# Performance work log

Measured on AMD Instinct MI355X. Metric: run time of the kernel, lower is better.

Reference implementation:

```python
import jax, jax.numpy as jnp
import numpy as np

B, S, H, L, V = 128, 512, 1024, 4, 32000


def setup_inputs() -> dict:
    key = jax.random.key(0)
    ks = jax.random.split(key, 7)
    lengths = jax.random.randint(ks[0], (B,), 1, S + 1)
    lengths = lengths.at[0].set(S)  # force max length == S so T is static
    tok = jax.random.randint(ks[1], (B, S), 1, V)  # nonzero tokens inside length
    pos = jnp.arange(S)[None, :]
    x = jnp.where(pos < lengths[:, None], tok, 0)  # 0 = pad (x>0 defines length)
    emb = jax.random.normal(ks[2], (V, H), dtype=jnp.float32) * 0.02
    W_ih = jax.random.normal(ks[3], (L, 4 * H, H), dtype=jnp.float32) / np.float32(np.sqrt(H))
    W_hh = jax.random.normal(ks[4], (L, 4 * H, H), dtype=jnp.float32) / np.float32(np.sqrt(H))
    b_ih = jax.random.normal(ks[5], (L, 4 * H), dtype=jnp.float32) * 0.01
    b_hh = jax.random.normal(ks[6], (L, 4 * H), dtype=jnp.float32) * 0.01
    return {"x": x, "emb": emb, "W_ih": W_ih, "W_hh": W_hh, "b_ih": b_ih, "b_hh": b_hh}


def reference(x, emb, W_ih, W_hh, b_ih, b_hh):
    # lengths and pack's descending sort (pack_padded_sequence, enforce_sorted=False)
    lengths = jnp.sum(x > 0, axis=1)                         # [B]
    sorted_idx = jnp.argsort(-lengths, stable=True)          # sorted (desc) order
    unsort_idx = jnp.argsort(sorted_idx)                     # packed.unsorted_indices

    # Source bug: `start` is never advanced, so every iteration runs a ONE-step
    # stacked LSTM (zero init state) on packed.data[0:bs_t] == t=0 embeddings of
    # the bs_t longest sequences. Compute that single step once on all rows.
    xt = emb[x[sorted_idx, 0]]                               # [B, H] sorted order
    h0 = jnp.zeros_like(xt)                                  # zero initial hidden
    hs, cs = [], []
    for l in range(W_ih.shape[0]):
        gates = xt @ W_ih[l].T + b_ih[l] + h0 @ W_hh[l].T + b_hh[l]
        i, f, g, o = jnp.split(gates, 4, axis=-1)            # torch LSTMCell order
        c = jax.nn.sigmoid(i) * jnp.tanh(g)                  # f * c0 = 0
        h = jax.nn.sigmoid(o) * jnp.tanh(c)
        xt = h
        hs.append(h)
        cs.append(c)

    # output[t, b] = top-layer h for original seq b, zeroed where t >= lengths[b]
    T = x.shape[1]                                           # max length == S
    h_top = xt[unsort_idx]                                   # back to original order
    tmask = (jnp.arange(T)[:, None] < lengths[None, :]).astype(h_top.dtype)  # [T,B]
    output = tmask[:, :, None] * h_top[None, :, :]           # [T, B, H]

    # state from the LAST loop iteration: sorted order, rows >= bs_last zero-padded
    bs_last = jnp.sum(lengths >= T)                          # batch size at t = T-1
    smask = (jnp.arange(x.shape[0]) < bs_last).astype(h_top.dtype)[None, :, None]
    state_h = jnp.stack(hs, axis=0) * smask                  # [L, B, H]
    state_c = jnp.stack(cs, axis=0) * smask                  # [L, B, H]
    return output, state_h, state_c
```

## Files before the change

kernel.cpp:

```cpp
#include <hip/hip_runtime.h>

#define Bn 128
#define Sn 512
#define Hn 1024
#define Ln 4

typedef float nfloat4 __attribute__((ext_vector_type(4)));

__device__ __forceinline__ float sigmoidf_(float x) { return 1.0f / (1.0f + __expf(-x)); }

__global__ __launch_bounds__(128) void len_kernel(const int* __restrict__ x, int* __restrict__ lengths) {
  const int b = blockIdx.x, t = threadIdx.x;
  int4 v = ((const int4*)x)[b * 128 + t];
  int c = (v.x > 0) + (v.y > 0) + (v.z > 0) + (v.w > 0);
  for (int off = 32; off > 0; off >>= 1) c += __shfl_down(c, off);
  __shared__ int tmp[2];
  if ((t & 63) == 0) tmp[t >> 6] = c;
  __syncthreads();
  if (t == 0) lengths[b] = tmp[0] + tmp[1];
}

__global__ __launch_bounds__(128) void sort_kernel(const int* __restrict__ x, const int* __restrict__ lengths,
                                                   int* __restrict__ rank, int* __restrict__ tok_sorted,
                                                   int* __restrict__ bs_last) {
  __shared__ int sl[128];
  __shared__ int cnt;
  const int b = threadIdx.x;
  const int len = lengths[b];
  sl[b] = len;
  if (b == 0) cnt = 0;
  __syncthreads();
  int r = 0;
  for (int b2 = 0; b2 < 128; b2++) {
    int l2 = sl[b2];
    r += (l2 > len) || (l2 == len && b2 < b);
  }
  rank[b] = r;
  tok_sorted[r] = x[b * Sn];
  if (len >= Sn) atomicAdd(&cnt, 1);
  __syncthreads();
  if (b == 0) bs_last[0] = cnt;
}

__global__ __launch_bounds__(256) void gather_kernel(const int* __restrict__ tok_sorted,
                                                     const float* __restrict__ emb,
                                                     float* __restrict__ xt0) {
  const int r = blockIdx.x;
  const int tok = tok_sorted[r];
  ((float4*)xt0)[r * 256 + threadIdx.x] = ((const float4*)emb)[(size_t)tok * 256 + threadIdx.x];
}

__global__ __launch_bounds__(256) void gemm_kernel(const float* __restrict__ xt,
                                                   const float* __restrict__ Wl,
                                                   float* __restrict__ part) {
  __shared__ float xtT[32][132];
  __shared__ float Ws[32][96];
  const int t = threadIdx.x;
  const int mtile = blockIdx.x & 31;
  const int kc = blockIdx.x >> 5;
  const int rg = t & 31;
  const int msub = t >> 5;
  const int k0 = kc * 128;

  float acc[3][4][4];
#pragma unroll
  for (int q = 0; q < 3; q++)
#pragma unroll
    for (int mm = 0; mm < 4; mm++)
#pragma unroll
      for (int rr = 0; rr < 4; rr++) acc[q][mm][rr] = 0.0f;

  float4 xreg[4], wreg[3];
  {
    const int kt = k0;
#pragma unroll
    for (int i = 0; i < 4; i++) {
      int vi = i * 256 + t, r = vi >> 3, kv = vi & 7;
      xreg[i] = *(const float4*)&xt[r * 1024 + kt + kv * 4];
    }
#pragma unroll
    for (int i = 0; i < 3; i++) {
      int vi = i * 256 + t, jj = vi >> 3, kv = vi & 7;
      int q = jj >> 5, mloc = jj & 31;
      int qoff = (q == 0) ? 0 : ((q == 1) ? 2048 : 3072);
      wreg[i] = *(const float4*)&Wl[(size_t)(qoff + mtile * 32 + mloc) * 1024 + kt + kv * 4];
    }
  }

#pragma unroll
  for (int tile = 0; tile < 4; tile++) {
    __syncthreads();
#pragma unroll
    for (int i = 0; i < 4; i++) {
      int vi = i * 256 + t, r = vi >> 3, kv = vi & 7;
      xtT[kv * 4 + 0][r] = xreg[i].x;
      xtT[kv * 4 + 1][r] = xreg[i].y;
      xtT[kv * 4 + 2][r] = xreg[i].z;
      xtT[kv * 4 + 3][r] = xreg[i].w;
    }
#pragma unroll
    for (int i = 0; i < 3; i++) {
      int vi = i * 256 + t, jj = vi >> 3, kv = vi & 7;
      Ws[kv * 4 + 0][jj] = wreg[i].x;
      Ws[kv * 4 + 1][jj] = wreg[i].y;
      Ws[kv * 4 + 2][jj] = wreg[i].z;
      Ws[kv * 4 + 3][jj] = wreg[i].w;
    }
    float4 xnxt[4], wnxt[3];
    if (tile < 3) {
      const int kt = k0 + (tile + 1) * 32;
#pragma unroll
      for (int i = 0; i < 4; i++) {
        int vi = i * 256 + t, r = vi >> 3, kv = vi & 7;
        xnxt[i] = *(const float4*)&xt[r * 1024 + kt + kv * 4];
      }
#pragma unroll
      for (int i = 0; i < 3; i++) {
        int vi = i * 256 + t, jj = vi >> 3, kv = vi & 7;
        int q = jj >> 5, mloc = jj & 31;
        int qoff = (q == 0) ? 0 : ((q == 1) ? 2048 : 3072);
        wnxt[i] = *(const float4*)&Wl[(size_t)(qoff + mtile * 32 + mloc) * 1024 + kt + kv * 4];
      }
    }
    __syncthreads();
#pragma unroll
    for (int kk = 0; kk < 32; kk++) {
      const float4 xv = *(const float4*)&xtT[kk][rg * 4];
      const float4 w0 = *(const float4*)&Ws[kk][msub * 4];
      const float4 w1 = *(const float4*)&Ws[kk][32 + msub * 4];
      const float4 w2 = *(const float4*)&Ws[kk][64 + msub * 4];
      const float xa[4] = {xv.x, xv.y, xv.z, xv.w};
      const float wv[3][4] = {{w0.x, w0.y, w0.z, w0.w},
                              {w1.x, w1.y, w1.z, w1.w},
                              {w2.x, w2.y, w2.z, w2.w}};
#pragma unroll
      for (int q = 0; q < 3; q++)
#pragma unroll
        for (int mm = 0; mm < 4; mm++)
#pragma unroll
          for (int rr = 0; rr < 4; rr++)
            acc[q][mm][rr] = fmaf(wv[q][mm], xa[rr], acc[q][mm][rr]);
    }
    if (tile < 3) {
#pragma unroll
      for (int i = 0; i < 4; i++) xreg[i] = xnxt[i];
#pragma unroll
      for (int i = 0; i < 3; i++) wreg[i] = wnxt[i];
    }
  }

  const int mbase = mtile * 32 + msub * 4;
#pragma unroll
  for (int q = 0; q < 3; q++)
#pragma unroll
    for (int mm = 0; mm < 4; mm++) {
      float4 v = make_float4(acc[q][mm][0], acc[q][mm][1], acc[q][mm][2], acc[q][mm][3]);
      *(float4*)&part[(((size_t)kc * 3 + q) * 1024 + (mbase + mm)) * 128 + rg * 4] = v;
    }
}

__global__ __launch_bounds__(256) void act_kernel(const float* __restrict__ part,
                                                  const float* __restrict__ bih,
                                                  const float* __restrict__ bhh,
                                                  const int* __restrict__ bs_last,
                                                  float* __restrict__ xt_out,
                                                  float* __restrict__ sh,
                                                  float* __restrict__ sc) {
  __shared__ float hT[128][17];
  __shared__ float cT[128][17];
  const int t = threadIdx.x;
  const int m0 = blockIdx.x * 16;
  const int bs = bs_last[0];
#pragma unroll
  for (int i = 0; i < 8; i++) {
    int e = i * 256 + t;
    int r = e & 127;
    int mloc = e >> 7;
    int m = m0 + mloc;
    float si = 0.f, sg = 0.f, so = 0.f;
#pragma unroll
    for (int kc = 0; kc < 8; kc++) {
      si += part[(((size_t)kc * 3 + 0) * 1024 + m) * 128 + r];
      sg += part[(((size_t)kc * 3 + 1) * 1024 + m) * 128 + r];
      so += part[(((size_t)kc * 3 + 2) * 1024 + m) * 128 + r];
    }
    si += bih[m] + bhh[m];
    sg += bih[2048 + m] + bhh[2048 + m];
    so += bih[3072 + m] + bhh[3072 + m];
    float c = sigmoidf_(si) * tanhf(sg);
    float h = sigmoidf_(so) * tanhf(c);
    hT[r][mloc] = h;
    cT[r][mloc] = c;
  }
  __syncthreads();
#pragma unroll
  for (int i = 0; i < 8; i++) {
    int e = i * 256 + t;
    int mloc = e & 15;
    int r = e >> 4;
    float h = hT[r][mloc];
    float c = cT[r][mloc];
    float msk = (r < bs) ? 1.0f : 0.0f;
    xt_out[r * 1024 + m0 + mloc] = h;
    sh[r * 1024 + m0 + mloc] = msk * h;
    sc[r * 1024 + m0 + mloc] = msk * c;
  }
}

__global__ __launch_bounds__(256) void bcast_kernel(const float* __restrict__ hfin,
                                                    const int* __restrict__ lengths,
                                                    const int* __restrict__ rank,
                                                    float* __restrict__ out) {
  const int b = blockIdx.x & 127;
  const int tp = blockIdx.x >> 7;
  const int len = lengths[b];
  nfloat4 v = (nfloat4)0.0f;
  if (tp < len) {
    const int r = rank[b];
    v = ((const nfloat4*)hfin)[r * 256 + threadIdx.x];
  }
  __builtin_nontemporal_store(v, &((nfloat4*)out)[(size_t)blockIdx.x * 256 + threadIdx.x]);
}

extern "C" void kernel_launch(void* const* d_in, const int* in_sizes, int n_in,
                              void* d_out, int out_size, void* d_ws, size_t ws_size,
                              hipStream_t stream) {
  const int* x = (const int*)d_in[0];
  const float* emb = (const float*)d_in[1];
  const float* W_ih = (const float*)d_in[2];
  const float* b_ih = (const float*)d_in[4];
  const float* b_hh = (const float*)d_in[5];

  float* out = (float*)d_out;
  float* sh = out + (size_t)Sn * Bn * Hn;
  float* sc = sh + (size_t)Ln * Bn * Hn;
  float* part = out;

  char* ws = (char*)d_ws;
  int* lengths = (int*)ws;
  int* rank = lengths + 128;
  int* tok_sorted = rank + 128;
  int* bs_last = tok_sorted + 128;
  float* xtA = (float*)(ws + 4096);
  float* xtB = xtA + 128 * 1024;

  len_kernel<<<128, 128, 0, stream>>>(x, lengths);
  sort_kernel<<<1, 128, 0, stream>>>(x, lengths, rank, tok_sorted, bs_last);
  gather_kernel<<<128, 256, 0, stream>>>(tok_sorted, emb, xtA);

  float* xin = xtA;
  float* xout = xtB;
  for (int l = 0; l < Ln; l++) {
    gemm_kernel<<<256, 256, 0, stream>>>(xin, W_ih + (size_t)l * 4 * Hn * Hn, part);
    act_kernel<<<64, 256, 0, stream>>>(part, b_ih + l * 4 * Hn, b_hh + l * 4 * Hn, bs_last,
                                       xout, sh + (size_t)l * Bn * Hn, sc + (size_t)l * Bn * Hn);
    float* tmp = xin; xin = xout; xout = tmp;
  }
  bcast_kernel<<<Sn * Bn, 256, 0, stream>>>(xin, lengths, rank, out);
}
```

Measured before the change: 521.2 us.

## Fuse embedding gather into first GEMM, simplify act kernel, coarsen broadcast

Drops the separate gather kernel: the first layer's GEMM reads embedding rows directly through a token index cached in shared memory. The activation kernel becomes one thread per batch row handling four hidden units, with float4 stores and no shared-memory transpose. The broadcast kernel goes from one block per (t,b) to 1024 blocks that each write 64 timesteps in a loop. Together these cut launch count and per-block overhead, at the cost of less parallelism per block in the act and broadcast kernels.

```diff
diff --git a/kernel.cpp b/kernel.cpp
--- a/kernel.cpp
+++ b/kernel.cpp
@@ -42,25 +42,32 @@
   if (b == 0) bs_last[0] = cnt;
 }
 
-__global__ __launch_bounds__(256) void gather_kernel(const int* __restrict__ tok_sorted,
-                                                     const float* __restrict__ emb,
-                                                     float* __restrict__ xt0) {
-  const int r = blockIdx.x;
-  const int tok = tok_sorted[r];
-  ((float4*)xt0)[r * 256 + threadIdx.x] = ((const float4*)emb)[(size_t)tok * 256 + threadIdx.x];
-}
-
 __global__ __launch_bounds__(256) void gemm_kernel(const float* __restrict__ xt,
+                                                   const int* __restrict__ tok,
                                                    const float* __restrict__ Wl,
                                                    float* __restrict__ part) {
   __shared__ float xtT[32][132];
   __shared__ float Ws[32][96];
+  __shared__ int sTok[128];
   const int t = threadIdx.x;
   const int mtile = blockIdx.x & 31;
   const int kc = blockIdx.x >> 5;
   const int rg = t & 31;
   const int msub = t >> 5;
   const int k0 = kc * 128;
+  const int kv4 = (t & 7) * 4;
+
+  if (tok != nullptr) {
+    if (t < 128) sTok[t] = tok[t];
+    __syncthreads();
+  }
+  const float* xrow[4];
+#pragma unroll
+  for (int i = 0; i < 4; i++) {
+    const int r = i * 32 + (t >> 3);
+    const int row = (tok != nullptr) ? sTok[r] : r;
+    xrow[i] = xt + (size_t)row * 1024;
+  }
 
   float acc[3][4][4];
 #pragma unroll
@@ -72,18 +79,14 @@
 
   float4 xreg[4], wreg[3];
   {
-    const int kt = k0;
-#pragma unroll
-    for (int i = 0; i < 4; i++) {
-      int vi = i * 256 + t, r = vi >> 3, kv = vi & 7;
-      xreg[i] = *(const float4*)&xt[r * 1024 + kt + kv * 4];
-    }
+#pragma unroll
+    for (int i = 0; i < 4; i++) xreg[i] = *(const float4*)&xrow[i][k0 + kv4];
 #pragma unroll
     for (int i = 0; i < 3; i++) {
-      int vi = i * 256 + t, jj = vi >> 3, kv = vi & 7;
+      int jj = i * 32 + (t >> 3);
       int q = jj >> 5, mloc = jj & 31;
       int qoff = (q == 0) ? 0 : ((q == 1) ? 2048 : 3072);
-      wreg[i] = *(const float4*)&Wl[(size_t)(qoff + mtile * 32 + mloc) * 1024 + kt + kv * 4];
+      wreg[i] = *(const float4*)&Wl[(size_t)(qoff + mtile * 32 + mloc) * 1024 + k0 + kv4];
     }
   }
 
@@ -92,34 +95,31 @@
     __syncthreads();
 #pragma unroll
     for (int i = 0; i < 4; i++) {
-      int vi = i * 256 + t, r = vi >> 3, kv = vi & 7;
-      xtT[kv * 4 + 0][r] = xreg[i].x;
-      xtT[kv * 4 + 1][r] = xreg[i].y;
-      xtT[kv * 4 + 2][r] = xreg[i].z;
-      xtT[kv * 4 + 3][r] = xreg[i].w;
+      const int r = i * 32 + (t >> 3);
+      xtT[kv4 + 0][r] = xreg[i].x;
+      xtT[kv4 + 1][r] = xreg[i].y;
+      xtT[kv4 + 2][r] = xreg[i].z;
+      xtT[kv4 + 3][r] = xreg[i].w;
     }
 #pragma unroll
     for (int i = 0; i < 3; i++) {
-      int vi = i * 256 + t, jj = vi >> 3, kv = vi & 7;
-      Ws[kv * 4 + 0][jj] = wreg[i].x;
-      Ws[kv * 4 + 1][jj] = wreg[i].y;
-      Ws[kv * 4 + 2][jj] = wreg[i].z;
-      Ws[kv * 4 + 3][jj] = wreg[i].w;
+      const int jj = i * 32 + (t >> 3);
+      Ws[kv4 + 0][jj] = wreg[i].x;
+      Ws[kv4 + 1][jj] = wreg[i].y;
+      Ws[kv4 + 2][jj] = wreg[i].z;
+      Ws[kv4 + 3][jj] = wreg[i].w;
     }
     float4 xnxt[4], wnxt[3];
     if (tile < 3) {
       const int kt = k0 + (tile + 1) * 32;
 #pragma unroll
-      for (int i = 0; i < 4; i++) {
-        int vi = i * 256 + t, r = vi >> 3, kv = vi & 7;
-        xnxt[i] = *(const float4*)&xt[r * 1024 + kt + kv * 4];
-      }
+      for (int i = 0; i < 4; i++) xnxt[i] = *(const float4*)&xrow[i][kt + kv4];
 #pragma unroll
       for (int i = 0; i < 3; i++) {
-        int vi = i * 256 + t, jj = vi >> 3, kv = vi & 7;
+        int jj = i * 32 + (t >> 3);
         int q = jj >> 5, mloc = jj & 31;
         int qoff = (q == 0) ? 0 : ((q == 1) ? 2048 : 3072);
-        wnxt[i] = *(const float4*)&Wl[(size_t)(qoff + mtile * 32 + mloc) * 1024 + kt + kv * 4];
+        wnxt[i] = *(const float4*)&Wl[(size_t)(qoff + mtile * 32 + mloc) * 1024 + kt + kv4];
       }
     }
     __syncthreads();
@@ -159,52 +159,42 @@
     }
 }
 
-__global__ __launch_bounds__(256) void act_kernel(const float* __restrict__ part,
+__global__ __launch_bounds__(128) void act_kernel(const float* __restrict__ part,
                                                   const float* __restrict__ bih,
                                                   const float* __restrict__ bhh,
                                                   const int* __restrict__ bs_last,
                                                   float* __restrict__ xt_out,
                                                   float* __restrict__ sh,
                                                   float* __restrict__ sc) {
-  __shared__ float hT[128][17];
-  __shared__ float cT[128][17];
-  const int t = threadIdx.x;
-  const int m0 = blockIdx.x * 16;
+  const int r = threadIdx.x;
+  const int m0 = blockIdx.x * 4;
   const int bs = bs_last[0];
-#pragma unroll
-  for (int i = 0; i < 8; i++) {
-    int e = i * 256 + t;
-    int r = e & 127;
-    int mloc = e >> 7;
-    int m = m0 + mloc;
+  float hv[4], cv[4];
+#pragma unroll
+  for (int mm = 0; mm < 4; mm++) {
+    const int m = m0 + mm;
     float si = 0.f, sg = 0.f, so = 0.f;
 #pragma unroll
     for (int kc = 0; kc < 8; kc++) {
-      si += part[(((size_t)kc * 3 + 0) * 1024 + m) * 128 + r];
-      sg += part[(((size_t)kc * 3 + 1) * 1024 + m) * 128 + r];
-      so += part[(((size_t)kc * 3 + 2) * 1024 + m) * 128 + r];
+      const float* p = part + (((size_t)kc * 3) * 1024 + m) * 128 + r;
+      si += p[0];
+      sg += p[(size_t)1024 * 128];
+      so += p[(size_t)2048 * 128];
     }
     si += bih[m] + bhh[m];
     sg += bih[2048 + m] + bhh[2048 + m];
     so += bih[3072 + m] + bhh[3072 + m];
-    float c = sigmoidf_(si) * tanhf(sg);
-    float h = sigmoidf_(so) * tanhf(c);
-    hT[r][mloc] = h;
-    cT[r][mloc] = c;
-  }
-  __syncthreads();
-#pragma unroll
-  for (int i = 0; i < 8; i++) {
-    int e = i * 256 + t;
-    int mloc = e & 15;
-    int r = e >> 4;
-    float h = hT[r][mloc];
-    float c = cT[r][mloc];
-    float msk = (r < bs) ? 1.0f : 0.0f;
-    xt_out[r * 1024 + m0 + mloc] = h;
-    sh[r * 1024 + m0 + mloc] = msk * h;
-    sc[r * 1024 + m0 + mloc] = msk * c;
-  }
+    const float c = sigmoidf_(si) * tanhf(sg);
+    const float h = sigmoidf_(so) * tanhf(c);
+    hv[mm] = h;
+    cv[mm] = c;
+  }
+  const float msk = (r < bs) ? 1.0f : 0.0f;
+  *(float4*)&xt_out[(size_t)r * 1024 + m0] = make_float4(hv[0], hv[1], hv[2], hv[3]);
+  *(float4*)&sh[(size_t)r * 1024 + m0] =
+      make_float4(msk * hv[0], msk * hv[1], msk * hv[2], msk * hv[3]);
+  *(float4*)&sc[(size_t)r * 1024 + m0] =
+      make_float4(msk * cv[0], msk * cv[1], msk * cv[2], msk * cv[3]);
 }
 
 __global__ __launch_bounds__(256) void bcast_kernel(const float* __restrict__ hfin,
@@ -212,14 +202,23 @@
                                                     const int* __restrict__ rank,
                                                     float* __restrict__ out) {
   const int b = blockIdx.x & 127;
-  const int tp = blockIdx.x >> 7;
+  const int c = blockIdx.x >> 7;
   const int len = lengths[b];
+  const int t0 = c * 64;
   nfloat4 v = (nfloat4)0.0f;
-  if (tp < len) {
-    const int r = rank[b];
-    v = ((const nfloat4*)hfin)[r * 256 + threadIdx.x];
-  }
-  __builtin_nontemporal_store(v, &((nfloat4*)out)[(size_t)blockIdx.x * 256 + threadIdx.x]);
+  if (t0 < len) v = ((const nfloat4*)hfin)[rank[b] * 256 + threadIdx.x];
+  int valid = len - t0;
+  valid = valid < 0 ? 0 : (valid > 64 ? 64 : valid);
+  nfloat4* p = (nfloat4*)out + ((size_t)t0 * 128 + b) * 256 + threadIdx.x;
+  for (int i = 0; i < valid; i++) {
+    __builtin_nontemporal_store(v, p);
+    p += 32768;
+  }
+  const nfloat4 z = (nfloat4)0.0f;
+  for (int i = valid; i < 64; i++) {
+    __builtin_nontemporal_store(z, p);
+    p += 32768;
+  }
 }
 
 extern "C" void kernel_launch(void* const* d_in, const int* in_sizes, int n_in,
@@ -246,15 +245,17 @@
 
   len_kernel<<<128, 128, 0, stream>>>(x, lengths);
   sort_kernel<<<1, 128, 0, stream>>>(x, lengths, rank, tok_sorted, bs_last);
-  gather_kernel<<<128, 256, 0, stream>>>(tok_sorted, emb, xtA);
-
-  float* xin = xtA;
-  float* xout = xtB;
+
+  float* bufs[2] = {xtA, xtB};
+  const float* xin = emb;
+  const int* tokp = tok_sorted;
   for (int l = 0; l < Ln; l++) {
-    gemm_kernel<<<256, 256, 0, stream>>>(xin, W_ih + (size_t)l * 4 * Hn * Hn, part);
-    act_kernel<<<64, 256, 0, stream>>>(part, b_ih + l * 4 * Hn, b_hh + l * 4 * Hn, bs_last,
-                                       xout, sh + (size_t)l * Bn * Hn, sc + (size_t)l * Bn * Hn);
-    float* tmp = xin; xin = xout; xout = tmp;
-  }
-  bcast_kernel<<<Sn * Bn, 256, 0, stream>>>(xin, lengths, rank, out);
-}
+    gemm_kernel<<<256, 256, 0, stream>>>(xin, tokp, W_ih + (size_t)l * 4 * Hn * Hn, part);
+    act_kernel<<<256, 128, 0, stream>>>(part, b_ih + l * 4 * Hn, b_hh + l * 4 * Hn, bs_last,
+                                        bufs[l & 1], sh + (size_t)l * Bn * Hn,
+                                        sc + (size_t)l * Bn * Hn);
+    xin = bufs[l & 1];
+    tokp = nullptr;
+  }
+  bcast_kernel<<<1024, 256, 0, stream>>>(xin, lengths, rank, out);
+}
```

Result: faster. 494.9 us (-5.0%).
